# Kernel tuning notes

Measured on AMD Instinct MI355X. Metric: run time of the kernel, lower is better.

## Reference

```python
import jax, jax.numpy as jnp
import numpy as np

USER_NUM = 100000
ITEM_NUM = 50000
N = USER_NUM + ITEM_NUM
EMB = 64
N_LAYERS = 3
N_EDGES = 8000000
EPS = 0.1


def setup_inputs() -> dict:
    key = jax.random.key(0)
    ks = jax.random.split(key, 8)
    return {
        "user_emb": jax.random.normal(ks[0], (USER_NUM, EMB), dtype=jnp.float32),
        "item_emb": jax.random.normal(ks[1], (ITEM_NUM, EMB), dtype=jnp.float32),
        "user_prototypes": jax.random.normal(ks[2], (4000, EMB), dtype=jnp.float32),
        "item_prototypes": jax.random.normal(ks[3], (4000, EMB), dtype=jnp.float32),
        "adj_rows": jax.random.randint(ks[4], (N_EDGES,), 0, N, dtype=jnp.int64)
        if jax.config.jax_enable_x64 else jax.random.randint(ks[4], (N_EDGES,), 0, N, dtype=jnp.int32),
        "adj_cols": jax.random.randint(ks[5], (N_EDGES,), 0, N, dtype=jnp.int64)
        if jax.config.jax_enable_x64 else jax.random.randint(ks[5], (N_EDGES,), 0, N, dtype=jnp.int32),
        "adj_vals": jax.random.uniform(ks[6], (N_EDGES,), dtype=jnp.float32),
        "noise": jax.random.uniform(ks[7], (N_LAYERS, N, EMB), dtype=jnp.float32),
    }


def _spmm(rows, cols, vals, x):
    # sparse [N,N] @ dense [N,EMB] via gather + segment-sum
    return jax.ops.segment_sum(vals[:, None] * x[cols], rows, num_segments=N)


def _l2_normalize(x, eps=1e-12):
    # matches torch F.normalize(dim=-1)
    nrm = jnp.sqrt(jnp.sum(x * x, axis=-1, keepdims=True))
    return x / jnp.maximum(nrm, eps)


def reference(user_emb, item_emb, user_prototypes, item_prototypes,
              adj_rows, adj_cols, adj_vals, noise):
    # perturbed=True path (noise injection each layer)
    ego = jnp.concatenate([user_emb, item_emb], axis=0)  # [N, EMB]
    acc = jnp.zeros_like(ego)
    for k in range(N_LAYERS):
        ego = _spmm(adj_rows, adj_cols, adj_vals, ego)
        ego = ego + jnp.sign(ego) * _l2_normalize(noise[k]) * EPS
        acc = acc + ego
    all_embeddings = acc / N_LAYERS  # mean over stacked layers
    user_all = all_embeddings[:USER_NUM]
    item_all = all_embeddings[USER_NUM:]
    return (user_all, item_all, user_prototypes, item_prototypes)
```

## Files before the change

### kernel.cpp

```cpp
#include <hip/hip_runtime.h>

#define USER_NUM 100000
#define ITEM_NUM 50000
#define NN (USER_NUM + ITEM_NUM)
#define EMB 64
#define N_EDGES 8000000
#define EPS_C 0.1f
#define PROTO 4000

#define BSHIFT 6
#define BROWS 64
#define NB ((NN + BROWS - 1) / BROWS)
#define NSUB 8
#define CAPS 608
#define WIN (NSUB * CAPS)
#define CAP 4608

#define SBSHIFT 9
#define SBROWS 512
#define NSB ((NN + SBROWS - 1) / SBROWS)
#define SCAP 28160
#define SF_STRIDE 16
#define CHS 4096
#define NCH ((N_EDGES + CHS - 1) / CHS)
#define RITER (CHS / 4 / 256)

static __device__ __forceinline__ unsigned short f32_to_bf16_rne(float f) {
    unsigned u = __float_as_uint(f);
    u += 0x7FFFu + ((u >> 16) & 1u);
    return (unsigned short)(u >> 16);
}
static __device__ __forceinline__ float bf16_to_f32(unsigned short h) {
    return __uint_as_float(((unsigned)h) << 16);
}
static __device__ __forceinline__ float bf16_lo(unsigned u) {
    return __uint_as_float(u << 16);
}
static __device__ __forceinline__ float bf16_hi(unsigned u) {
    return __uint_as_float(u & 0xFFFF0000u);
}
static __device__ __forceinline__ unsigned pack_bf16(float lo, float hi) {
    return (unsigned)f32_to_bf16_rne(lo) | ((unsigned)f32_to_bf16_rne(hi) << 16);
}

__global__ __launch_bounds__(256) void concat_bf16_kernel(const float* __restrict__ u,
                                                          const float* __restrict__ it,
                                                          unsigned short* __restrict__ out) {
    long i4 = (long)blockIdx.x * 256 + threadIdx.x;
    const long usz4 = (long)USER_NUM * EMB / 4;
    const long tot4 = (long)NN * EMB / 4;
    if (i4 >= tot4) return;
    const float4* src = (i4 < usz4) ? (const float4*)u : (const float4*)it;
    long j = (i4 < usz4) ? i4 : (i4 - usz4);
    float4 v = src[j];
    ushort4 o;
    o.x = f32_to_bf16_rne(v.x); o.y = f32_to_bf16_rne(v.y);
    o.z = f32_to_bf16_rne(v.z); o.w = f32_to_bf16_rne(v.w);
    ((ushort4*)out)[i4] = o;
}

__global__ __launch_bounds__(256) void chunk_sort_scatter(const int* __restrict__ rows,
                                                          const int* __restrict__ cols,
                                                          const float* __restrict__ vals,
                                                          int* __restrict__ sfill,
                                                          uint2* __restrict__ sbuf) {
    __shared__ uint2 buf[CHS];
    __shared__ unsigned short binid[CHS];
    __shared__ int hist[NSB];
    __shared__ int pref[NSB + 1];
    __shared__ int gbase[NSB];
    __shared__ int fill[NSB];

    const int tid   = threadIdx.x;
    const int start = blockIdx.x * CHS;
    const int n     = (start + CHS <= N_EDGES) ? CHS : (N_EDGES - start);
    const int n4    = n >> 2;

    for (int b = tid; b < NSB; b += 256) { hist[b] = 0; fill[b] = 0; }
    __syncthreads();

    int4 rloc[RITER];
    const int4* rows4 = (const int4*)(rows + start);
    {
        int it = 0;
        for (int i = tid; i < n4; i += 256, ++it) {
            int4 r = rows4[i];
            rloc[it] = r;
            atomicAdd(&hist[r.x >> SBSHIFT], 1);
            atomicAdd(&hist[r.y >> SBSHIFT], 1);
            atomicAdd(&hist[r.z >> SBSHIFT], 1);
            atomicAdd(&hist[r.w >> SBSHIFT], 1);
        }
    }
    __syncthreads();

    if (tid < 64) {
        int carry = 0;
        #pragma unroll
        for (int g = 0; g < (NSB + 63) / 64; ++g) {
            int idx = g * 64 + tid;
            int h = (idx < NSB) ? hist[idx] : 0;
            int v = h;
            #pragma unroll
            for (int off = 1; off < 64; off <<= 1) {
                int t = __shfl_up(v, off, 64);
                if (tid >= off) v += t;
            }
            if (idx < NSB) pref[idx] = carry + v - h;
            carry += __shfl(v, 63, 64);
        }
        if (tid == 0) pref[NSB] = carry;
    }
    __syncthreads();

    for (int b = tid; b < NSB; b += 256)
        gbase[b] = hist[b] ? atomicAdd(&sfill[b * SF_STRIDE], hist[b]) : 0;

    const int4*   cols4 = (const int4*)(cols + start);
    const float4* vals4 = (const float4*)(vals + start);
    {
        int it = 0;
        for (int i = tid; i < n4; i += 256, ++it) {
            int4   r = rloc[it];
            int4   c = cols4[i];
            float4 v = vals4[i];
            {
                int b = r.x >> SBSHIFT; int p = pref[b] + atomicAdd(&fill[b], 1);
                buf[p] = make_uint2(((unsigned)r.x & (SBROWS - 1)) | ((unsigned)c.x << SBSHIFT),
                                    __float_as_uint(v.x));
                binid[p] = (unsigned short)b;
            }
            {
                int b = r.y >> SBSHIFT; int p = pref[b] + atomicAdd(&fill[b], 1);
                buf[p] = make_uint2(((unsigned)r.y & (SBROWS - 1)) | ((unsigned)c.y << SBSHIFT),
                                    __float_as_uint(v.y));
                binid[p] = (unsigned short)b;
            }
            {
                int b = r.z >> SBSHIFT; int p = pref[b] + atomicAdd(&fill[b], 1);
                buf[p] = make_uint2(((unsigned)r.z & (SBROWS - 1)) | ((unsigned)c.z << SBSHIFT),
                                    __float_as_uint(v.z));
                binid[p] = (unsigned short)b;
            }
            {
                int b = r.w >> SBSHIFT; int p = pref[b] + atomicAdd(&fill[b], 1);
                buf[p] = make_uint2(((unsigned)r.w & (SBROWS - 1)) | ((unsigned)c.w << SBSHIFT),
                                    __float_as_uint(v.w));
                binid[p] = (unsigned short)b;
            }
        }
    }
    __syncthreads();

    for (int j = tid; j < n; j += 256) {
        int b = binid[j];
        int g = gbase[b] + (j - pref[b]);
        if (g < SCAP) sbuf[(size_t)b * SCAP + g] = buf[j];
    }
}

__global__ __launch_bounds__(512) void bin_rowsort(const int* __restrict__ sfill,
                                                   const uint2* __restrict__ sbuf,
                                                   uint2* __restrict__ dst,
                                                   int* __restrict__ row_start,
                                                   int* __restrict__ row_cnt) {
    __shared__ int hist[SBROWS], pref[SBROWS], fill[SBROWS];
    const int s = blockIdx.x, tid = threadIdx.x;
    int total = sfill[s * SF_STRIDE]; if (total > SCAP) total = SCAP;
    const uint2* src = sbuf + (size_t)s * SCAP;

    for (int r = tid; r < SBROWS; r += 512) { hist[r] = 0; fill[r] = 0; }
    __syncthreads();

    const int n2 = total >> 1;
    const uint4* src4 = (const uint4*)src;
    for (int i = tid; i < n2; i += 512) {
        uint4 q = src4[i];
        atomicAdd(&hist[q.x & (SBROWS - 1)], 1);
        atomicAdd(&hist[q.z & (SBROWS - 1)], 1);
    }
    if (tid == 0 && (total & 1)) atomicAdd(&hist[src[total - 1].x & (SBROWS - 1)], 1);
    __syncthreads();

    if (tid < 64) {
        int carry = 0;
        #pragma unroll
        for (int g = 0; g < SBROWS / 64; ++g) {
            int idx = g * 64 + tid;
            int h = hist[idx];
            int v = h;
            #pragma unroll
            for (int off = 1; off < 64; off <<= 1) {
                int t = __shfl_up(v, off, 64);
                if (tid >= off) v += t;
            }
            pref[idx] = carry + v - h;
            carry += __shfl(v, 63, 64);
        }
    }
    __syncthreads();

    uint2* dwin = dst + (size_t)s * SCAP;
    for (int i = tid; i < n2; i += 512) {
        uint4 q = src4[i];
        {
            int r = (int)(q.x & (SBROWS - 1));
            int p = pref[r] + atomicAdd(&fill[r], 1);
            uint2 o; o.x = q.x >> SBSHIFT; o.y = q.y;
            dwin[p] = o;
        }
        {
            int r = (int)(q.z & (SBROWS - 1));
            int p = pref[r] + atomicAdd(&fill[r], 1);
            uint2 o; o.x = q.z >> SBSHIFT; o.y = q.w;
            dwin[p] = o;
        }
    }
    if (tid == 0 && (total & 1)) {
        uint2 pk = src[total - 1];
        int r = (int)(pk.x & (SBROWS - 1));
        int p = pref[r] + atomicAdd(&fill[r], 1);
        uint2 o; o.x = pk.x >> SBSHIFT; o.y = pk.y;
        dwin[p] = o;
    }
    if (tid < SBROWS) {
        int row = s * SBROWS + tid;
        if (row < NN) { row_start[row] = s * SCAP + pref[tid]; row_cnt[row] = hist[tid]; }
    }
}

__global__ __launch_bounds__(256) void spmm_csr_fused(const int* __restrict__ row_start,
                                                      const int* __restrict__ row_cnt,
                                                      const uint2* __restrict__ csr,
                                                      const unsigned short* __restrict__ x,
                                                      const float* __restrict__ noise_k,
                                                      unsigned short* __restrict__ ego_out,
                                                      float* __restrict__ acc,
                                                      int mode) {
    int row  = (blockIdx.x * 256 + threadIdx.x) >> 6;
    int lane = threadIdx.x & 63;
    if (row >= NN) return;
    const int slot = lane >> 3;
    const int m    = lane & 7;
    const unsigned moff = (unsigned)m << 3;

    int s   = row_start[row];
    int end = s + row_cnt[row];

    float a0 = 0.f, a1 = 0.f, a2 = 0.f, a3 = 0.f;
    float a4 = 0.f, a5 = 0.f, a6 = 0.f, a7 = 0.f;
    float b0 = 0.f, b1 = 0.f, b2 = 0.f, b3 = 0.f;
    float b4 = 0.f, b5 = 0.f, b6 = 0.f, b7 = 0.f;
    int e = s;
    for (; e + 16 <= end; e += 16) {
        uint2 pA = csr[e + slot];
        uint2 pB = csr[e + 8 + slot];
        uint4 gA = *(const uint4*)(x + (((unsigned)pA.x) << 6) + moff);
        uint4 gB = *(const uint4*)(x + (((unsigned)pB.x) << 6) + moff);
        float vA = __uint_as_float(pA.y);
        float vB = __uint_as_float(pB.y);
        a0 += vA * bf16_lo(gA.x); a1 += vA * bf16_hi(gA.x);
        a2 += vA * bf16_lo(gA.y); a3 += vA * bf16_hi(gA.y);
        a4 += vA * bf16_lo(gA.z); a5 += vA * bf16_hi(gA.z);
        a6 += vA * bf16_lo(gA.w); a7 += vA * bf16_hi(gA.w);
        b0 += vB * bf16_lo(gB.x); b1 += vB * bf16_hi(gB.x);
        b2 += vB * bf16_lo(gB.y); b3 += vB * bf16_hi(gB.y);
        b4 += vB * bf16_lo(gB.z); b5 += vB * bf16_hi(gB.z);
        b6 += vB * bf16_lo(gB.w); b7 += vB * bf16_hi(gB.w);
    }
    for (; e < end; e += 8) {
        int idx = e + slot;
        uint2 p = make_uint2(0u, 0u);
        if (idx < end) p = csr[idx];
        uint4 g = *(const uint4*)(x + (((unsigned)p.x) << 6) + moff);
        float v = __uint_as_float(p.y);
        a0 += v * bf16_lo(g.x); a1 += v * bf16_hi(g.x);
        a2 += v * bf16_lo(g.y); a3 += v * bf16_hi(g.y);
        a4 += v * bf16_lo(g.z); a5 += v * bf16_hi(g.z);
        a6 += v * bf16_lo(g.w); a7 += v * bf16_hi(g.w);
    }
    a0 += b0; a1 += b1; a2 += b2; a3 += b3;
    a4 += b4; a5 += b5; a6 += b6; a7 += b7;

    #pragma unroll
    for (int off = 8; off < 64; off <<= 1) {
        a0 += __shfl_xor(a0, off, 64);
        a1 += __shfl_xor(a1, off, 64);
        a2 += __shfl_xor(a2, off, 64);
        a3 += __shfl_xor(a3, off, 64);
        a4 += __shfl_xor(a4, off, 64);
        a5 += __shfl_xor(a5, off, 64);
        a6 += __shfl_xor(a6, off, 64);
        a7 += __shfl_xor(a7, off, 64);
    }

    if (slot == 0) {
        size_t base4 = (size_t)row * 16 + ((unsigned)m << 1);
        float4 n0 = ((const float4*)noise_k)[base4];
        float4 n1 = ((const float4*)noise_k)[base4 + 1];
        float ss = n0.x * n0.x + n0.y * n0.y + n0.z * n0.z + n0.w * n0.w
                 + n1.x * n1.x + n1.y * n1.y + n1.z * n1.z + n1.w * n1.w;
        #pragma unroll
        for (int off = 1; off < 8; off <<= 1) ss += __shfl_xor(ss, off, 64);
        float inv = EPS_C / fmaxf(sqrtf(ss), 1e-12f);

        float e0 = fmaf(((a0 > 0.f) ? 1.f : ((a0 < 0.f) ? -1.f : 0.f)) * n0.x, inv, a0);
        float e1 = fmaf(((a1 > 0.f) ? 1.f : ((a1 < 0.f) ? -1.f : 0.f)) * n0.y, inv, a1);
        float e2 = fmaf(((a2 > 0.f) ? 1.f : ((a2 < 0.f) ? -1.f : 0.f)) * n0.z, inv, a2);
        float e3 = fmaf(((a3 > 0.f) ? 1.f : ((a3 < 0.f) ? -1.f : 0.f)) * n0.w, inv, a3);
        float e4 = fmaf(((a4 > 0.f) ? 1.f : ((a4 < 0.f) ? -1.f : 0.f)) * n1.x, inv, a4);
        float e5 = fmaf(((a5 > 0.f) ? 1.f : ((a5 < 0.f) ? -1.f : 0.f)) * n1.y, inv, a5);
        float e6 = fmaf(((a6 > 0.f) ? 1.f : ((a6 < 0.f) ? -1.f : 0.f)) * n1.z, inv, a6);
        float e7 = fmaf(((a7 > 0.f) ? 1.f : ((a7 < 0.f) ? -1.f : 0.f)) * n1.w, inv, a7);

        uint4 o;
        o.x = pack_bf16(e0, e1); o.y = pack_bf16(e2, e3);
        o.z = pack_bf16(e4, e5); o.w = pack_bf16(e6, e7);
        ((uint4*)ego_out)[(size_t)row * 8 + m] = o;

        float4* accp = (float4*)acc + base4;
        if (mode == 0) {
            accp[0] = make_float4(e0, e1, e2, e3);
            accp[1] = make_float4(e4, e5, e6, e7);
        } else if (mode == 1) {
            float4 c0 = accp[0], c1 = accp[1];
            c0.x += e0; c0.y += e1; c0.z += e2; c0.w += e3;
            c1.x += e4; c1.y += e5; c1.z += e6; c1.w += e7;
            accp[0] = c0; accp[1] = c1;
        } else {
            float4 c0 = accp[0], c1 = accp[1];
            c0.x = (c0.x + e0) * (1.0f / 3.0f); c0.y = (c0.y + e1) * (1.0f / 3.0f);
            c0.z = (c0.z + e2) * (1.0f / 3.0f); c0.w = (c0.w + e3) * (1.0f / 3.0f);
            c1.x = (c1.x + e4) * (1.0f / 3.0f); c1.y = (c1.y + e5) * (1.0f / 3.0f);
            c1.z = (c1.z + e6) * (1.0f / 3.0f); c1.w = (c1.w + e7) * (1.0f / 3.0f);
            accp[0] = c0; accp[1] = c1;
        }
    }
}

__global__ __launch_bounds__(256) void bucket_scatter_fixed(const int* __restrict__ rows,
                                                            const int* __restrict__ cols,
                                                            const float* __restrict__ vals,
                                                            int* __restrict__ bfill,
                                                            uint2* __restrict__ bbuf) {
    int e = blockIdx.x * 256 + threadIdx.x;
    if (e >= N_EDGES) return;
    int sub = blockIdx.x & (NSUB - 1);
    int r = rows[e];
    int b = r >> BSHIFT;
    int pos = atomicAdd(&bfill[b * NSUB + sub], 1);
    if (pos < CAPS) {
        uint2 pk;
        pk.x = (unsigned)(r & (BROWS - 1)) | ((unsigned)cols[e] << BSHIFT);
        pk.y = __float_as_uint(vals[e]);
        bbuf[(size_t)b * WIN + sub * CAPS + pos] = pk;
    }
}

__global__ __launch_bounds__(256) void bucket_sort_fixed(const int* __restrict__ bfill,
                                                         uint2* __restrict__ bbuf,
                                                         int* __restrict__ row_start,
                                                         int* __restrict__ row_cnt) {
    __shared__ uint2 buf[CAP];
    __shared__ int scnt[NSUB], soff[NSUB];
    __shared__ int h[BROWS], pref[BROWS], fill[BROWS];
    int b = blockIdx.x;
    int tid = threadIdx.x;
    if (tid < NSUB) {
        int c = bfill[b * NSUB + tid];
        scnt[tid] = (c < CAPS) ? c : CAPS;
    }
    if (tid < BROWS) { h[tid] = 0; fill[tid] = 0; }
    __syncthreads();
    if (tid == 0) {
        int run = 0;
        #pragma unroll
        for (int s = 0; s < NSUB; ++s) { soff[s] = run; run += scnt[s]; }
    }
    __syncthreads();
    int total = soff[NSUB - 1] + scnt[NSUB - 1];
    if (total > CAP) total = CAP;
    for (int s = 0; s < NSUB; ++s) {
        int c = scnt[s], off = soff[s];
        const uint2* src = bbuf + (size_t)b * WIN + s * CAPS;
        for (int i = tid; i < c; i += 256)
            if (off + i < CAP) buf[off + i] = src[i];
    }
    __syncthreads();
    for (int i = tid; i < total; i += 256) atomicAdd(&h[buf[i].x & (BROWS - 1)], 1);
    __syncthreads();
    if (tid == 0) {
        int run = 0;
        #pragma unroll
        for (int r = 0; r < BROWS; ++r) { pref[r] = run; run += h[r]; }
    }
    __syncthreads();
    uint2* dst = bbuf + (size_t)b * WIN;
    for (int i = tid; i < total; i += 256) {
        unsigned m = buf[i].x;
        int rl = (int)(m & (BROWS - 1));
        int pos = pref[rl] + atomicAdd(&fill[rl], 1);
        uint2 pk;
        pk.x = m >> BSHIFT;
        pk.y = buf[i].y;
        dst[pos] = pk;
    }
    if (tid < BROWS) {
        int row = b * BROWS + tid;
        if (row < NN) { row_start[row] = b * WIN + pref[tid]; row_cnt[row] = h[tid]; }
    }
}

__global__ __launch_bounds__(256) void spmm_csr_old(const int* __restrict__ row_start,
                                                    const int* __restrict__ row_cnt,
                                                    const uint2* __restrict__ csr,
                                                    const unsigned short* __restrict__ x,
                                                    const float* __restrict__ noise_k,
                                                    unsigned short* __restrict__ ego_out,
                                                    float* __restrict__ acc,
                                                    int mode) {
    int row = (blockIdx.x * 256 + threadIdx.x) >> 6;
    int lane = threadIdx.x & 63;
    if (row >= NN) return;
    int s = row_start[row];
    int end = s + row_cnt[row];
    float a0 = 0.f, a1 = 0.f, a2 = 0.f, a3 = 0.f;
    int e = s;
    for (; e + 4 <= end; e += 4) {
        uint2 p0 = csr[e], p1 = csr[e + 1], p2 = csr[e + 2], p3 = csr[e + 3];
        a0 += __uint_as_float(p0.y) * bf16_to_f32(x[(size_t)p0.x * EMB + lane]);
        a1 += __uint_as_float(p1.y) * bf16_to_f32(x[(size_t)p1.x * EMB + lane]);
        a2 += __uint_as_float(p2.y) * bf16_to_f32(x[(size_t)p2.x * EMB + lane]);
        a3 += __uint_as_float(p3.y) * bf16_to_f32(x[(size_t)p3.x * EMB + lane]);
    }
    for (; e < end; ++e) {
        uint2 p = csr[e];
        a0 += __uint_as_float(p.y) * bf16_to_f32(x[(size_t)p.x * EMB + lane]);
    }
    float a = (a0 + a1) + (a2 + a3);
    size_t idx = (size_t)row * EMB + lane;
    float nv = noise_k[idx];
    float ss = nv * nv;
    #pragma unroll
    for (int off = 32; off >= 1; off >>= 1) ss += __shfl_xor(ss, off, 64);
    float nrm = fmaxf(sqrtf(ss), 1e-12f);
    float sgn = (a > 0.0f) ? 1.0f : ((a < 0.0f) ? -1.0f : 0.0f);
    float e1 = a + sgn * (nv / nrm) * EPS_C;
    ego_out[idx] = f32_to_bf16_rne(e1);
    if (mode == 0)      acc[idx] = e1;
    else if (mode == 1) acc[idx] += e1;
    else                acc[idx] = (acc[idx] + e1) * (1.0f / 3.0f);
}

__global__ __launch_bounds__(256) void concat_f32_kernel(const float* __restrict__ u,
                                                         const float* __restrict__ it,
                                                         float* __restrict__ out) {
    long i = (long)blockIdx.x * 256 + threadIdx.x;
    const long usz = (long)USER_NUM * EMB;
    const long tot = (long)NN * EMB;
    if (i >= tot) return;
    out[i] = (i < usz) ? u[i] : it[i - usz];
}

__global__ __launch_bounds__(256) void spmm_atomic_kernel(const int* __restrict__ rows,
                                                          const int* __restrict__ cols,
                                                          const float* __restrict__ vals,
                                                          const float* __restrict__ x,
                                                          float* __restrict__ y) {
    long t = (long)blockIdx.x * 256 + threadIdx.x;
    int e = (int)(t >> 6);
    int lane = (int)(t & 63);
    if (e >= N_EDGES) return;
    atomicAdd(&y[(long)rows[e] * EMB + lane], vals[e] * x[(long)cols[e] * EMB + lane]);
}

__global__ __launch_bounds__(256) void noise_acc_kernel(float* __restrict__ ego,
                                                        const float* __restrict__ noise_k,
                                                        float* __restrict__ acc,
                                                        int mode) {
    long t = (long)blockIdx.x * 256 + threadIdx.x;
    int node = (int)(t >> 6);
    int lane = (int)(t & 63);
    if (node >= NN) return;
    long idx = (long)node * EMB + lane;
    float nv = noise_k[idx];
    float s = nv * nv;
    #pragma unroll
    for (int off = 32; off >= 1; off >>= 1) s += __shfl_xor(s, off, 64);
    float nrm = fmaxf(sqrtf(s), 1e-12f);
    float e0 = ego[idx];
    float sgn = (e0 > 0.0f) ? 1.0f : ((e0 < 0.0f) ? -1.0f : 0.0f);
    float e1 = e0 + sgn * (nv / nrm) * EPS_C;
    ego[idx] = e1;
    if (mode == 0)      acc[idx] = e1;
    else if (mode == 1) acc[idx] += e1;
    else                acc[idx] = (acc[idx] + e1) * (1.0f / 3.0f);
}

extern "C" void kernel_launch(void* const* d_in, const int* in_sizes, int n_in,
                              void* d_out, int out_size, void* d_ws, size_t ws_size,
                              hipStream_t stream) {
    const float* user_emb   = (const float*)d_in[0];
    const float* item_emb   = (const float*)d_in[1];
    const float* user_proto = (const float*)d_in[2];
    const float* item_proto = (const float*)d_in[3];
    const int*   rows       = (const int*)d_in[4];
    const int*   cols       = (const int*)d_in[5];
    const float* vals       = (const float*)d_in[6];
    const float* noise      = (const float*)d_in[7];
    float* out = (float*)d_out;

    const size_t EGO_BF = ((size_t)NN * EMB * sizeof(unsigned short) + 255) & ~(size_t)255;
    const size_t NARR   = ((size_t)NN * sizeof(int) + 255) & ~(size_t)255;

    const size_t SBUF_SZ  = (size_t)NSB * SCAP * sizeof(uint2);
    const size_t DST_SZ   = (size_t)NSB * SCAP * sizeof(uint2);
    const size_t SFILL_SZ = ((size_t)NSB * SF_STRIDE * sizeof(int) + 255) & ~(size_t)255;
    const size_t required_new = 2 * EGO_BF + SBUF_SZ + DST_SZ + 2 * NARR + SFILL_SZ;

    const size_t BBUF   = (size_t)NB * WIN * sizeof(uint2);
    const size_t FARR   = ((size_t)NB * NSUB * sizeof(int) + 255) & ~(size_t)255;
    const size_t required_old = 2 * EGO_BF + BBUF + 2 * NARR + FARR;

    float* acc = out;
    const int elemTotal  = NN * EMB;
    const int elemBlocks = (elemTotal + 255) / 256;
    const int vecBlocks  = (elemTotal / 4 + 255) / 256;
    const int edgeBlocks = (N_EDGES + 255) / 256;
    const int rowWaveBlocks = (NN + 3) / 4;

    if (ws_size >= required_new) {
        char* p = (char*)d_ws;
        unsigned short* egoA = (unsigned short*)p;  p += EGO_BF;
        unsigned short* egoB = (unsigned short*)p;  p += EGO_BF;
        uint2* sbuf          = (uint2*)p;           p += SBUF_SZ;
        uint2* dstbuf        = (uint2*)p;           p += DST_SZ;
        int* row_start       = (int*)p;             p += NARR;
        int* row_cnt         = (int*)p;             p += NARR;
        int* sfill           = (int*)p;             p += SFILL_SZ;

        concat_bf16_kernel<<<vecBlocks, 256, 0, stream>>>(user_emb, item_emb, egoA);
        hipMemsetAsync(sfill, 0, (size_t)NSB * SF_STRIDE * sizeof(int), stream);
        chunk_sort_scatter<<<NCH, 256, 0, stream>>>(rows, cols, vals, sfill, sbuf);
        bin_rowsort<<<NSB, 512, 0, stream>>>(sfill, sbuf, dstbuf, row_start, row_cnt);

        unsigned short* cur = egoA;
        unsigned short* nxt = egoB;
        for (int k = 0; k < 3; ++k) {
            int mode = (k == 0) ? 0 : ((k == 2) ? 2 : 1);
            spmm_csr_fused<<<rowWaveBlocks, 256, 0, stream>>>(
                row_start, row_cnt, dstbuf, cur,
                noise + (size_t)k * NN * EMB, nxt, acc, mode);
            unsigned short* t = cur; cur = nxt; nxt = t;
        }
    } else if (ws_size >= required_old) {
        char* p = (char*)d_ws;
        unsigned short* egoA = (unsigned short*)p;  p += EGO_BF;
        unsigned short* egoB = (unsigned short*)p;  p += EGO_BF;
        uint2* bbuf          = (uint2*)p;           p += BBUF;
        int* row_start       = (int*)p;             p += NARR;
        int* row_cnt         = (int*)p;             p += NARR;
        int* bfill           = (int*)p;             p += FARR;

        concat_bf16_kernel<<<vecBlocks, 256, 0, stream>>>(user_emb, item_emb, egoA);
        hipMemsetAsync(bfill, 0, (size_t)NB * NSUB * sizeof(int), stream);
        bucket_scatter_fixed<<<edgeBlocks, 256, 0, stream>>>(rows, cols, vals, bfill, bbuf);
        bucket_sort_fixed<<<NB, 256, 0, stream>>>(bfill, bbuf, row_start, row_cnt);

        unsigned short* cur = egoA;
        unsigned short* nxt = egoB;
        for (int k = 0; k < 3; ++k) {
            int mode = (k == 0) ? 0 : ((k == 2) ? 2 : 1);
            spmm_csr_old<<<rowWaveBlocks, 256, 0, stream>>>(
                row_start, row_cnt, bbuf, cur,
                noise + (size_t)k * NN * EMB, nxt, acc, mode);
            unsigned short* t = cur; cur = nxt; nxt = t;
        }
    } else {
        const size_t EGO_SZ = (size_t)NN * EMB * sizeof(float);
        float* fA = (float*)d_ws;
        float* fB = (float*)((char*)d_ws + EGO_SZ);
        concat_f32_kernel<<<elemBlocks, 256, 0, stream>>>(user_emb, item_emb, fA);
        float* cur = fA; float* nxt = fB;
        for (int k = 0; k < 3; ++k) {
            hipMemsetAsync(nxt, 0, EGO_SZ, stream);
            spmm_atomic_kernel<<<N_EDGES / 4, 256, 0, stream>>>(rows, cols, vals, cur, nxt);
            int mode = (k == 0) ? 0 : ((k == 2) ? 2 : 1);
            noise_acc_kernel<<<elemBlocks, 256, 0, stream>>>(
                nxt, noise + (size_t)k * NN * EMB, acc, mode);
            float* t = cur; cur = nxt; nxt = t;
        }
    }

    hipMemcpyAsync(out + (size_t)NN * EMB, user_proto,
                   (size_t)PROTO * EMB * sizeof(float), hipMemcpyDeviceToDevice, stream);
    hipMemcpyAsync(out + (size_t)NN * EMB + (size_t)PROTO * EMB, item_proto,
                   (size_t)PROTO * EMB * sizeof(float), hipMemcpyDeviceToDevice, stream);
}
```

Measured before the change: 836.9 us.

## Replace global atomic bin offsets with per-chunk histogram and scan pass

Adds a separate histogram kernel and a per-bin prefix scan across chunks, so each chunk gets fixed write offsets instead of reserving them with global atomicAdd on sfill. This removes atomic contention and makes edge placement deterministic and ordered by chunk within each bin, which may help later row sorting and locality. The cost is an extra full read of the rows array, two extra launches, and a chunk-by-bin histogram buffer held in the workspace.

Measured after the change: 838.8 us. No clear change (+0.2%).

```diff
diff --git a/kernel.cpp b/kernel.cpp
--- a/kernel.cpp
+++ b/kernel.cpp
@@ -59,10 +59,52 @@
     ((ushort4*)out)[i4] = o;
 }
 
+__global__ __launch_bounds__(256) void chunk_hist(const int* __restrict__ rows,
+                                                  int* __restrict__ histc) {
+    __shared__ int hist[NSB];
+    const int c = blockIdx.x, tid = threadIdx.x;
+    const int start = c * CHS;
+    const int n = (start + CHS <= N_EDGES) ? CHS : (N_EDGES - start);
+    const int n4 = n >> 2;
+    for (int b = tid; b < NSB; b += 256) hist[b] = 0;
+    __syncthreads();
+    const int4* rows4 = (const int4*)(rows + start);
+    for (int i = tid; i < n4; i += 256) {
+        int4 r = rows4[i];
+        atomicAdd(&hist[r.x >> SBSHIFT], 1);
+        atomicAdd(&hist[r.y >> SBSHIFT], 1);
+        atomicAdd(&hist[r.z >> SBSHIFT], 1);
+        atomicAdd(&hist[r.w >> SBSHIFT], 1);
+    }
+    __syncthreads();
+    for (int b = tid; b < NSB; b += 256) histc[(size_t)c * NSB + b] = hist[b];
+}
+
+__global__ __launch_bounds__(256) void bin_scan(int* __restrict__ histc,
+                                                int* __restrict__ sfill) {
+    int wave = (blockIdx.x * 256 + threadIdx.x) >> 6;
+    int lane = threadIdx.x & 63;
+    if (wave >= NSB) return;
+    int running = 0;
+    for (int i0 = 0; i0 < NCH; i0 += 64) {
+        int idx = i0 + lane;
+        int v = (idx < NCH) ? histc[(size_t)idx * NSB + wave] : 0;
+        int incl = v;
+        #pragma unroll
+        for (int off = 1; off < 64; off <<= 1) {
+            int t = __shfl_up(incl, off, 64);
+            if (lane >= off) incl += t;
+        }
+        if (idx < NCH) histc[(size_t)idx * NSB + wave] = running + incl - v;
+        running += __shfl(incl, 63, 64);
+    }
+    if (lane == 0) sfill[wave * SF_STRIDE] = running;
+}
+
 __global__ __launch_bounds__(256) void chunk_sort_scatter(const int* __restrict__ rows,
                                                           const int* __restrict__ cols,
                                                           const float* __restrict__ vals,
-                                                          int* __restrict__ sfill,
+                                                          const int* __restrict__ offc,
                                                           uint2* __restrict__ sbuf) {
     __shared__ uint2 buf[CHS];
     __shared__ unsigned short binid[CHS];
@@ -76,7 +118,10 @@
     const int n     = (start + CHS <= N_EDGES) ? CHS : (N_EDGES - start);
     const int n4    = n >> 2;
 
-    for (int b = tid; b < NSB; b += 256) { hist[b] = 0; fill[b] = 0; }
+    for (int b = tid; b < NSB; b += 256) {
+        hist[b] = 0; fill[b] = 0;
+        gbase[b] = offc[(size_t)blockIdx.x * NSB + b];
+    }
     __syncthreads();
 
     int4 rloc[RITER];
@@ -112,9 +157,6 @@
         if (tid == 0) pref[NSB] = carry;
     }
     __syncthreads();
-
-    for (int b = tid; b < NSB; b += 256)
-        gbase[b] = hist[b] ? atomicAdd(&sfill[b * SF_STRIDE], hist[b]) : 0;
 
     const int4*   cols4 = (const int4*)(cols + start);
     const float4* vals4 = (const float4*)(vals + start);
@@ -323,17 +365,17 @@
             accp[0] = make_float4(e0, e1, e2, e3);
             accp[1] = make_float4(e4, e5, e6, e7);
         } else if (mode == 1) {
-            float4 c0 = accp[0], c1 = accp[1];
-            c0.x += e0; c0.y += e1; c0.z += e2; c0.w += e3;
-            c1.x += e4; c1.y += e5; c1.z += e6; c1.w += e7;
-            accp[0] = c0; accp[1] = c1;
+            float4 q0 = accp[0], q1 = accp[1];
+            q0.x += e0; q0.y += e1; q0.z += e2; q0.w += e3;
+            q1.x += e4; q1.y += e5; q1.z += e6; q1.w += e7;
+            accp[0] = q0; accp[1] = q1;
         } else {
-            float4 c0 = accp[0], c1 = accp[1];
-            c0.x = (c0.x + e0) * (1.0f / 3.0f); c0.y = (c0.y + e1) * (1.0f / 3.0f);
-            c0.z = (c0.z + e2) * (1.0f / 3.0f); c0.w = (c0.w + e3) * (1.0f / 3.0f);
-            c1.x = (c1.x + e4) * (1.0f / 3.0f); c1.y = (c1.y + e5) * (1.0f / 3.0f);
-            c1.z = (c1.z + e6) * (1.0f / 3.0f); c1.w = (c1.w + e7) * (1.0f / 3.0f);
-            accp[0] = c0; accp[1] = c1;
+            float4 q0 = accp[0], q1 = accp[1];
+            q0.x = (q0.x + e0) * (1.0f / 3.0f); q0.y = (q0.y + e1) * (1.0f / 3.0f);
+            q0.z = (q0.z + e2) * (1.0f / 3.0f); q0.w = (q0.w + e3) * (1.0f / 3.0f);
+            q1.x = (q1.x + e4) * (1.0f / 3.0f); q1.y = (q1.y + e5) * (1.0f / 3.0f);
+            q1.z = (q1.z + e6) * (1.0f / 3.0f); q1.w = (q1.w + e7) * (1.0f / 3.0f);
+            accp[0] = q0; accp[1] = q1;
         }
     }
 }
@@ -516,7 +558,8 @@
     const size_t SBUF_SZ  = (size_t)NSB * SCAP * sizeof(uint2);
     const size_t DST_SZ   = (size_t)NSB * SCAP * sizeof(uint2);
     const size_t SFILL_SZ = ((size_t)NSB * SF_STRIDE * sizeof(int) + 255) & ~(size_t)255;
-    const size_t required_new = 2 * EGO_BF + SBUF_SZ + DST_SZ + 2 * NARR + SFILL_SZ;
+    const size_t HISTC_SZ = ((size_t)NCH * NSB * sizeof(int) + 255) & ~(size_t)255;
+    const size_t required_new = 2 * EGO_BF + SBUF_SZ + DST_SZ + 2 * NARR + SFILL_SZ + HISTC_SZ;
 
     const size_t BBUF   = (size_t)NB * WIN * sizeof(uint2);
     const size_t FARR   = ((size_t)NB * NSUB * sizeof(int) + 255) & ~(size_t)255;
@@ -528,6 +571,7 @@
     const int vecBlocks  = (elemTotal / 4 + 255) / 256;
     const int edgeBlocks = (N_EDGES + 255) / 256;
     const int rowWaveBlocks = (NN + 3) / 4;
+    const int scanBlocks = (NSB + 3) / 4;
 
     if (ws_size >= required_new) {
         char* p = (char*)d_ws;
@@ -538,10 +582,12 @@
         int* row_start       = (int*)p;             p += NARR;
         int* row_cnt         = (int*)p;             p += NARR;
         int* sfill           = (int*)p;             p += SFILL_SZ;
+        int* histc           = (int*)p;             p += HISTC_SZ;
 
         concat_bf16_kernel<<<vecBlocks, 256, 0, stream>>>(user_emb, item_emb, egoA);
-        hipMemsetAsync(sfill, 0, (size_t)NSB * SF_STRIDE * sizeof(int), stream);
-        chunk_sort_scatter<<<NCH, 256, 0, stream>>>(rows, cols, vals, sfill, sbuf);
+        chunk_hist<<<NCH, 256, 0, stream>>>(rows, histc);
+        bin_scan<<<scanBlocks, 256, 0, stream>>>(histc, sfill);
+        chunk_sort_scatter<<<NCH, 256, 0, stream>>>(rows, cols, vals, histc, sbuf);
         bin_rowsort<<<NSB, 512, 0, stream>>>(sfill, sbuf, dstbuf, row_start, row_cnt);
 
         unsigned short* cur = egoA;
```
